# Performance work log

Hardware: AMD Instinct MI355X
Metric: run time of the kernel (lower is better)

Reference implementation:

```python
import jax, jax.numpy as jnp
import numpy as np

B, T, C, H, RANK = 4, 2048, 1024, 16, 8


def _lora_linear(x, W, b, A, Bm):
    # loralib-style: y = x W^T + b + (x A^T) B^T  (scaling alpha/r = 1)
    return x @ W.T + b + (x @ A.T) @ Bm.T


def setup_inputs() -> dict:
    key = jax.random.key(0)
    ks = jax.random.split(key, 6)
    s_in = 1.0 / np.sqrt(C)
    return {
        "x": jax.random.normal(ks[0], (B, T, C), jnp.float32),
        "c_attn_w": jax.random.normal(ks[1], (3 * C, C), jnp.float32) * s_in,
        "c_attn_b": jnp.zeros((3 * C,), jnp.float32),
        "c_attn_A": jax.random.normal(ks[2], (RANK, C), jnp.float32) * s_in,
        "c_attn_B": jnp.zeros((3 * C, RANK), jnp.float32),
        "c_proj_w": jax.random.normal(ks[3], (C, C), jnp.float32) * s_in,
        "c_proj_b": jnp.zeros((C,), jnp.float32),
        "c_proj_A": jax.random.normal(ks[4], (RANK, C), jnp.float32) * s_in,
        "c_proj_B": jnp.zeros((C, RANK), jnp.float32),
        "n_head": H,
    }


def reference(x, c_attn_w, c_attn_b, c_attn_A, c_attn_B,
              c_proj_w, c_proj_b, c_proj_A, c_proj_B, n_head):
    Bsz, Tlen, Cd = x.shape
    d = Cd // n_head
    qkv = _lora_linear(x, c_attn_w, c_attn_b, c_attn_A, c_attn_B)  # [B,T,3C]
    q, k, v = jnp.split(qkv, 3, axis=2)
    query, key_out = q, k  # returned pre-reshape, as in torch
    # [B, H, T, d]
    qh = q.reshape(Bsz, Tlen, n_head, d).transpose(0, 2, 1, 3)
    kh = k.reshape(Bsz, Tlen, n_head, d).transpose(0, 2, 1, 3)
    vh = v.reshape(Bsz, Tlen, n_head, d).transpose(0, 2, 1, 3)
    att = jnp.einsum('bhqd,bhkd->bhqk', qh, kh) * (1.0 / np.sqrt(d))
    causal = jnp.tril(jnp.ones((Tlen, Tlen), bool))
    att = jnp.where(causal[None, None], att, -jnp.inf)
    att = jax.nn.softmax(att, axis=-1)
    y = jnp.einsum('bhqk,bhkd->bhqd', att, vh)
    y = y.transpose(0, 2, 1, 3).reshape(Bsz, Tlen, Cd)
    out = _lora_linear(y, c_proj_w, c_proj_b, c_proj_A, c_proj_B)
    return out, query, key_out
```

## Files before the change

kernel.cpp:

```cpp
#include <hip/hip_runtime.h>
#include <stdint.h>

#define T_LEN 2048
#define C_DIM 1024
#define NHEAD 16
#define DHEAD 64
#define QOFF  8388608L
#define KOFF  16777216L
#define SCALE_LOG2 0.18033688011112042f

typedef float f32x4 __attribute__((ext_vector_type(4)));
typedef short bf16x8 __attribute__((ext_vector_type(8)));
typedef short s16x4 __attribute__((ext_vector_type(4)));
typedef unsigned short u16;

__device__ __forceinline__ float b2f(u16 h) {
  union { uint32_t u; float f; } v; v.u = ((uint32_t)h) << 16; return v.f;
}
__device__ __forceinline__ u16 f2b(float f) {
  union { float f; uint32_t u; } v; v.f = f;
  uint32_t r = v.u + 0x7fffu + ((v.u >> 16) & 1u);
  return (u16)(r >> 16);
}
__device__ __forceinline__ u16 f2b_tr(float f) {
  union { float f; uint32_t u; } v; v.f = f;
  return (u16)(v.u >> 16);
}
__device__ __forceinline__ void async16(const u16* g, u16* l) {
  __builtin_amdgcn_global_load_lds((const __attribute__((address_space(1))) void*)g,
                                   (__attribute__((address_space(3))) void*)l, 16, 0, 0);
}

#define MFMA16 __builtin_amdgcn_mfma_f32_16x16x32_bf16

__global__ __launch_bounds__(256) void convert_x(const float* __restrict__ xin,
                                                 u16* __restrict__ xc) {
  long i = ((long)blockIdx.x * 256 + threadIdx.x) * 4;
  f32x4 v = *(const f32x4*)(xin + i);
  s16x4 r;
  r[0] = (short)f2b(v[0]); r[1] = (short)f2b(v[1]);
  r[2] = (short)f2b(v[2]); r[3] = (short)f2b(v[3]);
  *(s16x4*)(xc + i) = r;
}

__global__ __launch_bounds__(256) void prep_weff(const float* __restrict__ W,
                                                 const float* __restrict__ Bm,
                                                 const float* __restrict__ Aw,
                                                 u16* __restrict__ out, int total) {
  int i = blockIdx.x * 256 + threadIdx.x;
  if (i >= total) return;
  int n = i >> 10, k = i & 1023;
  float acc = W[i];
#pragma unroll
  for (int r = 0; r < 8; r++) acc += Bm[n * 8 + r] * Aw[r * 1024 + k];
  out[i] = f2b(acc);
}

template <int MODE>
__global__ __launch_bounds__(256) void gemm_bt(const u16* __restrict__ A,
                                               const u16* __restrict__ Bt,
                                               const float* __restrict__ bias,
                                               float* __restrict__ outf,
                                               u16* __restrict__ kc,
                                               u16* __restrict__ vblk, int K) {
  __shared__ __align__(16) u16 ldsA[128 * 32];
  __shared__ __align__(16) u16 ldsB[128 * 32];
  const int t = threadIdx.x;
  const int lane = t & 63, l15 = lane & 15, quad = lane >> 4, w = t >> 6;
  const int wr = (w >> 1) * 64, wc = (w & 1) * 64;
  const long rowA = (long)blockIdx.y * 128;
  const long rowB = (long)blockIdx.x * 128;
  const int srow = t >> 2, scol = (t & 3) * 8;

  f32x4 acc[4][4];
#pragma unroll
  for (int i = 0; i < 4; i++)
#pragma unroll
    for (int j = 0; j < 4; j++) { f32x4 z = {0.f, 0.f, 0.f, 0.f}; acc[i][j] = z; }

  const u16* Ab = A + rowA * K;
  const u16* Bb = Bt + rowB * K;
  for (int k0 = 0; k0 < K; k0 += 32) {
    __syncthreads();
    async16(Ab + (long)srow * K + k0 + scol, &ldsA[t * 8]);
    async16(Ab + (long)(srow + 64) * K + k0 + scol, &ldsA[2048 + t * 8]);
    async16(Bb + (long)srow * K + k0 + scol, &ldsB[t * 8]);
    async16(Bb + (long)(srow + 64) * K + k0 + scol, &ldsB[2048 + t * 8]);
    __syncthreads();
    bf16x8 af[4], bfr[4];
#pragma unroll
    for (int g = 0; g < 4; g++) {
      af[g]  = *(const bf16x8*)&ldsA[(wr + g * 16 + l15) * 32 + quad * 8];
      bfr[g] = *(const bf16x8*)&ldsB[(wc + g * 16 + l15) * 32 + quad * 8];
    }
#pragma unroll
    for (int i = 0; i < 4; i++)
#pragma unroll
      for (int j = 0; j < 4; j++)
        acc[i][j] = MFMA16(af[i], bfr[j], acc[i][j], 0, 0, 0);
  }

#pragma unroll
  for (int i = 0; i < 4; i++) {
#pragma unroll
    for (int j = 0; j < 4; j++) {
      int n = (int)rowB + wc + j * 16 + l15;
      float bv = bias[n];
#pragma unroll
      for (int r = 0; r < 4; r++) {
        int m = (int)rowA + wr + i * 16 + quad * 4 + r;
        float val = acc[i][j][r] + bv;
        if constexpr (MODE == 1) {
          outf[(long)m * C_DIM + n] = val;
        } else {
          int sec = n >> 10;
          int nc = n & 1023;
          int h = nc >> 6, dd = nc & 63;
          int bb = m >> 11, tt = m & 2047;
          int bh = bb * NHEAD + h;
          if (sec == 0) {
            outf[QOFF + (long)m * C_DIM + nc] = val;
          } else if (sec == 1) {
            outf[KOFF + (long)m * C_DIM + nc] = val;
            kc[(long)bh * (T_LEN * 64) + (long)tt * 64 + dd] = f2b(val);
          } else {
            vblk[(long)bh * (T_LEN * 64) + (long)(tt >> 6) * 4096 + dd * 64 + (tt & 63)] = f2b(val);
          }
        }
      }
    }
  }
}

__global__ __launch_bounds__(256) void flash_attn(const float* __restrict__ qsec,
                                                  const u16* __restrict__ kc,
                                                  const u16* __restrict__ vblk,
                                                  u16* __restrict__ yb) {
  __shared__ __align__(16) u16 ldsK[2][64 * 64];
  __shared__ __align__(16) u16 ldsV[2][64 * 64];
  __shared__ __align__(16) u16 plds[4][32 * 72];
  const int t = threadIdx.x;
  const int lane = t & 63, l15 = lane & 15, quad = lane >> 4, w = t >> 6;
  const int qt = 15 - (blockIdx.x >> 6);
  const int bh = blockIdx.x & 63;
  const int q0 = qt * 128;
  const int bb = bh >> 4, h = bh & 15;

  const float* Qb = qsec + ((long)bb * T_LEN + q0 + w * 32) * C_DIM + h * DHEAD;
  bf16x8 qf[2][2];
#pragma unroll
  for (int rg = 0; rg < 2; rg++)
#pragma unroll
    for (int kk = 0; kk < 2; kk++) {
      const float* p = Qb + (long)(rg * 16 + l15) * C_DIM + kk * 32 + quad * 8;
      f32x4 a = *(const f32x4*)p, b = *(const f32x4*)(p + 4);
      bf16x8 r;
      r[0] = (short)f2b(a[0] * SCALE_LOG2); r[1] = (short)f2b(a[1] * SCALE_LOG2);
      r[2] = (short)f2b(a[2] * SCALE_LOG2); r[3] = (short)f2b(a[3] * SCALE_LOG2);
      r[4] = (short)f2b(b[0] * SCALE_LOG2); r[5] = (short)f2b(b[1] * SCALE_LOG2);
      r[6] = (short)f2b(b[2] * SCALE_LOG2); r[7] = (short)f2b(b[3] * SCALE_LOG2);
      qf[rg][kk] = r;
    }

  bf16x8 ones;
#pragma unroll
  for (int j = 0; j < 8; j++) ones[j] = (short)0x3F80;

  f32x4 o[2][4];
  f32x4 ls[2];
#pragma unroll
  for (int rg = 0; rg < 2; rg++) {
#pragma unroll
    for (int cg = 0; cg < 4; cg++) { f32x4 z = {0.f, 0.f, 0.f, 0.f}; o[rg][cg] = z; }
    f32x4 z = {0.f, 0.f, 0.f, 0.f}; ls[rg] = z;
  }

  const u16* kcb = kc + (long)bh * (T_LEN * 64);
  const u16* vbb = vblk + (long)bh * (T_LEN * 64);
  const int l0 = t, l1 = 256 + t;
  const int s0c = ((l0 >> 3) * 8 + ((l0 & 7) ^ ((l0 >> 3) & 7))) * 8;
  const int s1c = ((l1 >> 3) * 8 + ((l1 & 7) ^ ((l1 >> 3) & 7))) * 8;

  const int qminw = q0 + w * 32;
  const int nkt = (q0 + 128) >> 6;

#define KV_STAGE(kt_, b_) do {                                        \
    const u16* ks_ = kcb + (long)(kt_) * 4096;                        \
    const u16* vs_ = vbb + (long)(kt_) * 4096;                        \
    async16(ks_ + s0c, &ldsK[b_][l0 * 8]);                            \
    async16(ks_ + s1c, &ldsK[b_][l1 * 8]);                            \
    async16(vs_ + s0c, &ldsV[b_][l0 * 8]);                            \
    async16(vs_ + s1c, &ldsV[b_][l1 * 8]);                            \
  } while (0)

  KV_STAGE(0, 0);
  asm volatile("s_waitcnt vmcnt(0)" ::: "memory");
  __builtin_amdgcn_s_barrier();

  for (int kt = 0; kt < nkt; kt++) {
    const int kb0 = kt * 64;
    const int cur = kt & 1;
    if (kt + 1 < nkt) KV_STAGE(kt + 1, cur ^ 1);

    if (kb0 <= qminw + 31) {
      f32x4 s[2][4];
#pragma unroll
      for (int rg = 0; rg < 2; rg++)
#pragma unroll
        for (int kg = 0; kg < 4; kg++) { f32x4 z = {0.f, 0.f, 0.f, 0.f}; s[rg][kg] = z; }
#pragma unroll
      for (int kg = 0; kg < 4; kg++) {
        int row = kg * 16 + l15, sw = row & 7;
        bf16x8 kf0 = *(const bf16x8*)&ldsK[cur][row * 64 + ((quad ^ sw) * 8)];
        bf16x8 kf1 = *(const bf16x8*)&ldsK[cur][row * 64 + (((4 + quad) ^ sw) * 8)];
#pragma unroll
        for (int rg = 0; rg < 2; rg++) {
          s[rg][kg] = MFMA16(qf[rg][0], kf0, s[rg][kg], 0, 0, 0);
          s[rg][kg] = MFMA16(qf[rg][1], kf1, s[rg][kg], 0, 0, 0);
        }
      }
      const bool needMask = (kb0 + 63) > qminw;
#pragma unroll
      for (int rg = 0; rg < 2; rg++) {
#pragma unroll
        for (int r = 0; r < 4; r++) {
          float v0 = s[rg][0][r], v1 = s[rg][1][r], v2 = s[rg][2][r], v3 = s[rg][3][r];
          if (needMask) {
            int qrow = qminw + rg * 16 + quad * 4 + r;
            if (kb0 + l15 > qrow)      v0 = -3.0e38f;
            if (kb0 + 16 + l15 > qrow) v1 = -3.0e38f;
            if (kb0 + 32 + l15 > qrow) v2 = -3.0e38f;
            if (kb0 + 48 + l15 > qrow) v3 = -3.0e38f;
          }
          int prow = rg * 16 + quad * 4 + r;
          plds[w][prow * 72 + l15]      = f2b_tr(exp2f(v0));
          plds[w][prow * 72 + 16 + l15] = f2b_tr(exp2f(v1));
          plds[w][prow * 72 + 32 + l15] = f2b_tr(exp2f(v2));
          plds[w][prow * 72 + 48 + l15] = f2b_tr(exp2f(v3));
        }
      }
      asm volatile("s_waitcnt lgkmcnt(0)" ::: "memory");
      bf16x8 pf[2][2];
#pragma unroll
      for (int rg = 0; rg < 2; rg++)
#pragma unroll
        for (int kk = 0; kk < 2; kk++)
          pf[rg][kk] = *(const bf16x8*)&plds[w][(rg * 16 + l15) * 72 + kk * 32 + quad * 8];
#pragma unroll
      for (int rg = 0; rg < 2; rg++) {
        ls[rg] = MFMA16(pf[rg][0], ones, ls[rg], 0, 0, 0);
        ls[rg] = MFMA16(pf[rg][1], ones, ls[rg], 0, 0, 0);
      }
#pragma unroll
      for (int cg = 0; cg < 4; cg++) {
        int row = cg * 16 + l15, sw = row & 7;
        bf16x8 vf0 = *(const bf16x8*)&ldsV[cur][row * 64 + ((quad ^ sw) * 8)];
        bf16x8 vf1 = *(const bf16x8*)&ldsV[cur][row * 64 + (((4 + quad) ^ sw) * 8)];
#pragma unroll
        for (int rg = 0; rg < 2; rg++) {
          o[rg][cg] = MFMA16(pf[rg][0], vf0, o[rg][cg], 0, 0, 0);
          o[rg][cg] = MFMA16(pf[rg][1], vf1, o[rg][cg], 0, 0, 0);
        }
      }
    }

    asm volatile("s_waitcnt vmcnt(0)" ::: "memory");
    __builtin_amdgcn_s_barrier();
  }

#pragma unroll
  for (int rg = 0; rg < 2; rg++) {
#pragma unroll
    for (int r = 0; r < 4; r++) {
      float inv = 1.0f / ls[rg][r];
      int tt = q0 + w * 32 + rg * 16 + quad * 4 + r;
      long base = ((long)bb * T_LEN + tt) * C_DIM + h * DHEAD;
#pragma unroll
      for (int cg = 0; cg < 4; cg++)
        yb[base + cg * 16 + l15] = f2b(o[rg][cg][r] * inv);
    }
  }
}

extern "C" void kernel_launch(void* const* d_in, const int* in_sizes, int n_in,
                              void* d_out, int out_size, void* d_ws, size_t ws_size,
                              hipStream_t stream) {
  const float* x  = (const float*)d_in[0];
  const float* w1 = (const float*)d_in[1];
  const float* b1 = (const float*)d_in[2];
  const float* A1 = (const float*)d_in[3];
  const float* B1 = (const float*)d_in[4];
  const float* w2 = (const float*)d_in[5];
  const float* b2 = (const float*)d_in[6];
  const float* A2 = (const float*)d_in[7];
  const float* B2 = (const float*)d_in[8];
  float* outf = (float*)d_out;
  u16* outb16 = (u16*)d_out;

  u16* ws  = (u16*)d_ws;
  u16* w2e = ws;
  u16* w1e = ws + 1048576;
  u16* xc  = ws + 4194304;
  u16* yb  = ws + 1048576;
  u16* vblk = outb16;
  u16* kcp  = outb16 + 8388608;

  convert_x<<<8192, 256, 0, stream>>>(x, xc);
  prep_weff<<<12288, 256, 0, stream>>>(w1, B1, A1, w1e, 3072 * 1024);
  prep_weff<<<4096, 256, 0, stream>>>(w2, B2, A2, w2e, 1024 * 1024);
  gemm_bt<0><<<dim3(24, 64), 256, 0, stream>>>(xc, w1e, b1, outf, kcp, vblk, 1024);
  flash_attn<<<1024, 256, 0, stream>>>(outf + QOFF, kcp, vblk, yb);
  gemm_bt<1><<<dim3(8, 64), 256, 0, stream>>>(yb, w2e, b2, outf, nullptr, nullptr, 1024);
}
```

Measured before the change: 350.6 us.

## Pair causal q-tiles per attention block and fuse prep kernels into one launch

Each flash-attention block now processes two query tiles, p and 15-p, sequentially, so every block does the same amount of causal work. This halves the grid and removes the tail imbalance. The three preprocessing kernels (x conversion and the two LoRA weight merges) are merged into one launch to cut launch overhead. The trade-offs are fewer resident blocks for latency hiding and a serialized second pass per block.

```diff
diff --git a/kernel.cpp b/kernel.cpp
--- a/kernel.cpp
+++ b/kernel.cpp
@@ -33,27 +33,39 @@
 
 #define MFMA16 __builtin_amdgcn_mfma_f32_16x16x32_bf16
 
-__global__ __launch_bounds__(256) void convert_x(const float* __restrict__ xin,
-                                                 u16* __restrict__ xc) {
-  long i = ((long)blockIdx.x * 256 + threadIdx.x) * 4;
-  f32x4 v = *(const f32x4*)(xin + i);
-  s16x4 r;
-  r[0] = (short)f2b(v[0]); r[1] = (short)f2b(v[1]);
-  r[2] = (short)f2b(v[2]); r[3] = (short)f2b(v[3]);
-  *(s16x4*)(xc + i) = r;
-}
-
-__global__ __launch_bounds__(256) void prep_weff(const float* __restrict__ W,
-                                                 const float* __restrict__ Bm,
-                                                 const float* __restrict__ Aw,
-                                                 u16* __restrict__ out, int total) {
-  int i = blockIdx.x * 256 + threadIdx.x;
-  if (i >= total) return;
-  int n = i >> 10, k = i & 1023;
-  float acc = W[i];
-#pragma unroll
-  for (int r = 0; r < 8; r++) acc += Bm[n * 8 + r] * Aw[r * 1024 + k];
-  out[i] = f2b(acc);
+__global__ __launch_bounds__(256) void prep_all(const float* __restrict__ x,
+                                                u16* __restrict__ xc,
+                                                const float* __restrict__ w1,
+                                                const float* __restrict__ B1,
+                                                const float* __restrict__ A1,
+                                                u16* __restrict__ w1e,
+                                                const float* __restrict__ w2,
+                                                const float* __restrict__ B2,
+                                                const float* __restrict__ A2,
+                                                u16* __restrict__ w2e) {
+  int b = blockIdx.x;
+  if (b < 8192) {
+    long i = ((long)b * 256 + threadIdx.x) * 4;
+    f32x4 v = *(const f32x4*)(x + i);
+    s16x4 r;
+    r[0] = (short)f2b(v[0]); r[1] = (short)f2b(v[1]);
+    r[2] = (short)f2b(v[2]); r[3] = (short)f2b(v[3]);
+    *(s16x4*)(xc + i) = r;
+  } else if (b < 20480) {
+    int i = (b - 8192) * 256 + threadIdx.x;
+    int n = i >> 10, k = i & 1023;
+    float acc = w1[i];
+#pragma unroll
+    for (int r = 0; r < 8; r++) acc += B1[n * 8 + r] * A1[r * 1024 + k];
+    w1e[i] = f2b(acc);
+  } else {
+    int i = (b - 20480) * 256 + threadIdx.x;
+    int n = i >> 10, k = i & 1023;
+    float acc = w2[i];
+#pragma unroll
+    for (int r = 0; r < 8; r++) acc += B2[n * 8 + r] * A2[r * 1024 + k];
+    w2e[i] = f2b(acc);
+  }
 }
 
 template <int MODE>
@@ -141,48 +153,19 @@
   __shared__ __align__(16) u16 plds[4][32 * 72];
   const int t = threadIdx.x;
   const int lane = t & 63, l15 = lane & 15, quad = lane >> 4, w = t >> 6;
-  const int qt = 15 - (blockIdx.x >> 6);
+  const int p = blockIdx.x >> 6;
   const int bh = blockIdx.x & 63;
-  const int q0 = qt * 128;
   const int bb = bh >> 4, h = bh & 15;
 
-  const float* Qb = qsec + ((long)bb * T_LEN + q0 + w * 32) * C_DIM + h * DHEAD;
-  bf16x8 qf[2][2];
-#pragma unroll
-  for (int rg = 0; rg < 2; rg++)
-#pragma unroll
-    for (int kk = 0; kk < 2; kk++) {
-      const float* p = Qb + (long)(rg * 16 + l15) * C_DIM + kk * 32 + quad * 8;
-      f32x4 a = *(const f32x4*)p, b = *(const f32x4*)(p + 4);
-      bf16x8 r;
-      r[0] = (short)f2b(a[0] * SCALE_LOG2); r[1] = (short)f2b(a[1] * SCALE_LOG2);
-      r[2] = (short)f2b(a[2] * SCALE_LOG2); r[3] = (short)f2b(a[3] * SCALE_LOG2);
-      r[4] = (short)f2b(b[0] * SCALE_LOG2); r[5] = (short)f2b(b[1] * SCALE_LOG2);
-      r[6] = (short)f2b(b[2] * SCALE_LOG2); r[7] = (short)f2b(b[3] * SCALE_LOG2);
-      qf[rg][kk] = r;
-    }
-
   bf16x8 ones;
 #pragma unroll
   for (int j = 0; j < 8; j++) ones[j] = (short)0x3F80;
-
-  f32x4 o[2][4];
-  f32x4 ls[2];
-#pragma unroll
-  for (int rg = 0; rg < 2; rg++) {
-#pragma unroll
-    for (int cg = 0; cg < 4; cg++) { f32x4 z = {0.f, 0.f, 0.f, 0.f}; o[rg][cg] = z; }
-    f32x4 z = {0.f, 0.f, 0.f, 0.f}; ls[rg] = z;
-  }
 
   const u16* kcb = kc + (long)bh * (T_LEN * 64);
   const u16* vbb = vblk + (long)bh * (T_LEN * 64);
   const int l0 = t, l1 = 256 + t;
   const int s0c = ((l0 >> 3) * 8 + ((l0 & 7) ^ ((l0 >> 3) & 7))) * 8;
   const int s1c = ((l1 >> 3) * 8 + ((l1 & 7) ^ ((l1 >> 3) & 7))) * 8;
-
-  const int qminw = q0 + w * 32;
-  const int nkt = (q0 + 128) >> 6;
 
 #define KV_STAGE(kt_, b_) do {                                        \
     const u16* ks_ = kcb + (long)(kt_) * 4096;                        \
@@ -193,91 +176,125 @@
     async16(vs_ + s1c, &ldsV[b_][l1 * 8]);                            \
   } while (0)
 
-  KV_STAGE(0, 0);
-  asm volatile("s_waitcnt vmcnt(0)" ::: "memory");
-  __builtin_amdgcn_s_barrier();
-
-  for (int kt = 0; kt < nkt; kt++) {
-    const int kb0 = kt * 64;
-    const int cur = kt & 1;
-    if (kt + 1 < nkt) KV_STAGE(kt + 1, cur ^ 1);
-
-    if (kb0 <= qminw + 31) {
-      f32x4 s[2][4];
-#pragma unroll
-      for (int rg = 0; rg < 2; rg++)
-#pragma unroll
-        for (int kg = 0; kg < 4; kg++) { f32x4 z = {0.f, 0.f, 0.f, 0.f}; s[rg][kg] = z; }
-#pragma unroll
-      for (int kg = 0; kg < 4; kg++) {
-        int row = kg * 16 + l15, sw = row & 7;
-        bf16x8 kf0 = *(const bf16x8*)&ldsK[cur][row * 64 + ((quad ^ sw) * 8)];
-        bf16x8 kf1 = *(const bf16x8*)&ldsK[cur][row * 64 + (((4 + quad) ^ sw) * 8)];
-#pragma unroll
-        for (int rg = 0; rg < 2; rg++) {
-          s[rg][kg] = MFMA16(qf[rg][0], kf0, s[rg][kg], 0, 0, 0);
-          s[rg][kg] = MFMA16(qf[rg][1], kf1, s[rg][kg], 0, 0, 0);
-        }
+#pragma unroll 1
+  for (int half = 0; half < 2; half++) {
+    const int qt = half ? p : (15 - p);
+    const int q0 = qt * 128;
+
+    const float* Qb = qsec + ((long)bb * T_LEN + q0 + w * 32) * C_DIM + h * DHEAD;
+    bf16x8 qf[2][2];
+#pragma unroll
+    for (int rg = 0; rg < 2; rg++)
+#pragma unroll
+      for (int kk = 0; kk < 2; kk++) {
+        const float* ptr = Qb + (long)(rg * 16 + l15) * C_DIM + kk * 32 + quad * 8;
+        f32x4 a = *(const f32x4*)ptr, b = *(const f32x4*)(ptr + 4);
+        bf16x8 r;
+        r[0] = (short)f2b(a[0] * SCALE_LOG2); r[1] = (short)f2b(a[1] * SCALE_LOG2);
+        r[2] = (short)f2b(a[2] * SCALE_LOG2); r[3] = (short)f2b(a[3] * SCALE_LOG2);
+        r[4] = (short)f2b(b[0] * SCALE_LOG2); r[5] = (short)f2b(b[1] * SCALE_LOG2);
+        r[6] = (short)f2b(b[2] * SCALE_LOG2); r[7] = (short)f2b(b[3] * SCALE_LOG2);
+        qf[rg][kk] = r;
       }
-      const bool needMask = (kb0 + 63) > qminw;
-#pragma unroll
-      for (int rg = 0; rg < 2; rg++) {
-#pragma unroll
-        for (int r = 0; r < 4; r++) {
-          float v0 = s[rg][0][r], v1 = s[rg][1][r], v2 = s[rg][2][r], v3 = s[rg][3][r];
-          if (needMask) {
-            int qrow = qminw + rg * 16 + quad * 4 + r;
-            if (kb0 + l15 > qrow)      v0 = -3.0e38f;
-            if (kb0 + 16 + l15 > qrow) v1 = -3.0e38f;
-            if (kb0 + 32 + l15 > qrow) v2 = -3.0e38f;
-            if (kb0 + 48 + l15 > qrow) v3 = -3.0e38f;
-          }
-          int prow = rg * 16 + quad * 4 + r;
-          plds[w][prow * 72 + l15]      = f2b_tr(exp2f(v0));
-          plds[w][prow * 72 + 16 + l15] = f2b_tr(exp2f(v1));
-          plds[w][prow * 72 + 32 + l15] = f2b_tr(exp2f(v2));
-          plds[w][prow * 72 + 48 + l15] = f2b_tr(exp2f(v3));
-        }
-      }
-      asm volatile("s_waitcnt lgkmcnt(0)" ::: "memory");
-      bf16x8 pf[2][2];
-#pragma unroll
-      for (int rg = 0; rg < 2; rg++)
-#pragma unroll
-        for (int kk = 0; kk < 2; kk++)
-          pf[rg][kk] = *(const bf16x8*)&plds[w][(rg * 16 + l15) * 72 + kk * 32 + quad * 8];
-#pragma unroll
-      for (int rg = 0; rg < 2; rg++) {
-        ls[rg] = MFMA16(pf[rg][0], ones, ls[rg], 0, 0, 0);
-        ls[rg] = MFMA16(pf[rg][1], ones, ls[rg], 0, 0, 0);
-      }
-#pragma unroll
-      for (int cg = 0; cg < 4; cg++) {
-        int row = cg * 16 + l15, sw = row & 7;
-        bf16x8 vf0 = *(const bf16x8*)&ldsV[cur][row * 64 + ((quad ^ sw) * 8)];
-        bf16x8 vf1 = *(const bf16x8*)&ldsV[cur][row * 64 + (((4 + quad) ^ sw) * 8)];
-#pragma unroll
-        for (int rg = 0; rg < 2; rg++) {
-          o[rg][cg] = MFMA16(pf[rg][0], vf0, o[rg][cg], 0, 0, 0);
-          o[rg][cg] = MFMA16(pf[rg][1], vf1, o[rg][cg], 0, 0, 0);
-        }
-      }
-    }
-
+
+    f32x4 o[2][4];
+    f32x4 ls[2];
+#pragma unroll
+    for (int rg = 0; rg < 2; rg++) {
+#pragma unroll
+      for (int cg = 0; cg < 4; cg++) { f32x4 z = {0.f, 0.f, 0.f, 0.f}; o[rg][cg] = z; }
+      f32x4 z = {0.f, 0.f, 0.f, 0.f}; ls[rg] = z;
+    }
+
+    const int qminw = q0 + w * 32;
+    const int nkt = (q0 + 128) >> 6;
+
+    KV_STAGE(0, 0);
     asm volatile("s_waitcnt vmcnt(0)" ::: "memory");
     __builtin_amdgcn_s_barrier();
-  }
-
-#pragma unroll
-  for (int rg = 0; rg < 2; rg++) {
-#pragma unroll
-    for (int r = 0; r < 4; r++) {
-      float inv = 1.0f / ls[rg][r];
-      int tt = q0 + w * 32 + rg * 16 + quad * 4 + r;
-      long base = ((long)bb * T_LEN + tt) * C_DIM + h * DHEAD;
-#pragma unroll
-      for (int cg = 0; cg < 4; cg++)
-        yb[base + cg * 16 + l15] = f2b(o[rg][cg][r] * inv);
+
+    for (int kt = 0; kt < nkt; kt++) {
+      const int kb0 = kt * 64;
+      const int cur = kt & 1;
+      if (kt + 1 < nkt) KV_STAGE(kt + 1, cur ^ 1);
+
+      if (kb0 <= qminw + 31) {
+        f32x4 s[2][4];
+#pragma unroll
+        for (int rg = 0; rg < 2; rg++)
+#pragma unroll
+          for (int kg = 0; kg < 4; kg++) { f32x4 z = {0.f, 0.f, 0.f, 0.f}; s[rg][kg] = z; }
+#pragma unroll
+        for (int kg = 0; kg < 4; kg++) {
+          int row = kg * 16 + l15, sw = row & 7;
+          bf16x8 kf0 = *(const bf16x8*)&ldsK[cur][row * 64 + ((quad ^ sw) * 8)];
+          bf16x8 kf1 = *(const bf16x8*)&ldsK[cur][row * 64 + (((4 + quad) ^ sw) * 8)];
+#pragma unroll
+          for (int rg = 0; rg < 2; rg++) {
+            s[rg][kg] = MFMA16(qf[rg][0], kf0, s[rg][kg], 0, 0, 0);
+            s[rg][kg] = MFMA16(qf[rg][1], kf1, s[rg][kg], 0, 0, 0);
+          }
+        }
+        const bool needMask = (kb0 + 63) > qminw;
+#pragma unroll
+        for (int rg = 0; rg < 2; rg++) {
+#pragma unroll
+          for (int r = 0; r < 4; r++) {
+            float v0 = s[rg][0][r], v1 = s[rg][1][r], v2 = s[rg][2][r], v3 = s[rg][3][r];
+            if (needMask) {
+              int qrow = qminw + rg * 16 + quad * 4 + r;
+              if (kb0 + l15 > qrow)      v0 = -3.0e38f;
+              if (kb0 + 16 + l15 > qrow) v1 = -3.0e38f;
+              if (kb0 + 32 + l15 > qrow) v2 = -3.0e38f;
+              if (kb0 + 48 + l15 > qrow) v3 = -3.0e38f;
+            }
+            int prow = rg * 16 + quad * 4 + r;
+            plds[w][prow * 72 + l15]      = f2b_tr(exp2f(v0));
+            plds[w][prow * 72 + 16 + l15] = f2b_tr(exp2f(v1));
+            plds[w][prow * 72 + 32 + l15] = f2b_tr(exp2f(v2));
+            plds[w][prow * 72 + 48 + l15] = f2b_tr(exp2f(v3));
+          }
+        }
+        asm volatile("s_waitcnt lgkmcnt(0)" ::: "memory");
+        bf16x8 pf[2][2];
+#pragma unroll
+        for (int rg = 0; rg < 2; rg++)
+#pragma unroll
+          for (int kk = 0; kk < 2; kk++)
+            pf[rg][kk] = *(const bf16x8*)&plds[w][(rg * 16 + l15) * 72 + kk * 32 + quad * 8];
+#pragma unroll
+        for (int rg = 0; rg < 2; rg++) {
+          ls[rg] = MFMA16(pf[rg][0], ones, ls[rg], 0, 0, 0);
+          ls[rg] = MFMA16(pf[rg][1], ones, ls[rg], 0, 0, 0);
+        }
+#pragma unroll
+        for (int cg = 0; cg < 4; cg++) {
+          int row = cg * 16 + l15, sw = row & 7;
+          bf16x8 vf0 = *(const bf16x8*)&ldsV[cur][row * 64 + ((quad ^ sw) * 8)];
+          bf16x8 vf1 = *(const bf16x8*)&ldsV[cur][row * 64 + (((4 + quad) ^ sw) * 8)];
+#pragma unroll
+          for (int rg = 0; rg < 2; rg++) {
+            o[rg][cg] = MFMA16(pf[rg][0], vf0, o[rg][cg], 0, 0, 0);
+            o[rg][cg] = MFMA16(pf[rg][1], vf1, o[rg][cg], 0, 0, 0);
+          }
+        }
+      }
+
+      asm volatile("s_waitcnt vmcnt(0)" ::: "memory");
+      __builtin_amdgcn_s_barrier();
+    }
+
+#pragma unroll
+    for (int rg = 0; rg < 2; rg++) {
+#pragma unroll
+      for (int r = 0; r < 4; r++) {
+        float inv = 1.0f / ls[rg][r];
+        int tt = q0 + w * 32 + rg * 16 + quad * 4 + r;
+        long base = ((long)bb * T_LEN + tt) * C_DIM + h * DHEAD;
+#pragma unroll
+        for (int cg = 0; cg < 4; cg++)
+          yb[base + cg * 16 + l15] = f2b(o[rg][cg][r] * inv);
+      }
     }
   }
 }
@@ -305,10 +322,8 @@
   u16* vblk = outb16;
   u16* kcp  = outb16 + 8388608;
 
-  convert_x<<<8192, 256, 0, stream>>>(x, xc);
-  prep_weff<<<12288, 256, 0, stream>>>(w1, B1, A1, w1e, 3072 * 1024);
-  prep_weff<<<4096, 256, 0, stream>>>(w2, B2, A2, w2e, 1024 * 1024);
+  prep_all<<<24576, 256, 0, stream>>>(x, xc, w1, B1, A1, w1e, w2, B2, A2, w2e);
   gemm_bt<0><<<dim3(24, 64), 256, 0, stream>>>(xc, w1e, b1, outf, kcp, vblk, 1024);
-  flash_attn<<<1024, 256, 0, stream>>>(outf + QOFF, kcp, vblk, yb);
+  flash_attn<<<512, 256, 0, stream>>>(outf + QOFF, kcp, vblk, yb);
   gemm_bt<1><<<dim3(8, 64), 256, 0, stream>>>(yb, w2e, b2, outf, nullptr, nullptr, 1024);
 }
```

Measured after the change: 355.8 us. About the same (+1.5%).
